# Optimization experiments

Measured on AMD Instinct MI355X. Metric: run time of the kernel, lower is better.

The kernel has to match this reference:

```python
import jax, jax.numpy as jnp
import numpy as np

D_MODEL = 1024
N_HEADS = 16
HEAD_DIM = D_MODEL // N_HEADS


def setup_inputs() -> dict:
    key = jax.random.key(0)
    ks = jax.random.split(key, 9)
    s = 1.0 / np.sqrt(D_MODEL)
    x = jax.random.normal(ks[0], (2, 2048, D_MODEL), dtype=jnp.float32)
    Wq = jax.random.uniform(ks[1], (D_MODEL, D_MODEL), jnp.float32, -s, s)
    bq = jax.random.uniform(ks[2], (D_MODEL,), jnp.float32, -s, s)
    Wk = jax.random.uniform(ks[3], (D_MODEL, D_MODEL), jnp.float32, -s, s)
    bk = jax.random.uniform(ks[4], (D_MODEL,), jnp.float32, -s, s)
    Wv = jax.random.uniform(ks[5], (D_MODEL, D_MODEL), jnp.float32, -s, s)
    bv = jax.random.uniform(ks[6], (D_MODEL,), jnp.float32, -s, s)
    Wo = jax.random.uniform(ks[7], (D_MODEL, D_MODEL), jnp.float32, -s, s)
    bo = jax.random.uniform(ks[8], (D_MODEL,), jnp.float32, -s, s)
    return {"x": x, "Wq": Wq, "bq": bq, "Wk": Wk, "bk": bk,
            "Wv": Wv, "bv": bv, "Wo": Wo, "bo": bo}


def reference(x, Wq, bq, Wk, bk, Wv, bv, Wo, bo):
    B, S, _ = x.shape
    # project and split heads: [B, H, S, Dh]
    def heads(W, b):
        return (x @ W + b).reshape(B, S, N_HEADS, HEAD_DIM).transpose(0, 2, 1, 3)
    Q, K, V = heads(Wq, bq), heads(Wk, bk), heads(Wv, bv)
    scale = 1.0 / np.sqrt(HEAD_DIM).astype(np.float32)
    scores = jnp.einsum('bhsd,bhtd->bhst', Q, K) * scale  # [B,H,S,S]
    causal = jnp.tril(jnp.ones((S, S), dtype=bool))
    scores = jnp.where(causal, scores, -jnp.inf)
    attn = jax.nn.softmax(scores, axis=-1)
    out = jnp.einsum('bhst,bhtd->bhsd', attn, V)  # [B,H,S,Dh]
    out = out.transpose(0, 2, 1, 3).reshape(B, S, D_MODEL)
    return out @ Wo + bo
```

## Files before the change

kernel.cpp:

```cpp
#include <hip/hip_runtime.h>

typedef __attribute__((ext_vector_type(8))) __bf16 bfrag;
typedef __attribute__((ext_vector_type(4))) float f32x4;

#define MFMA(a, b, c) __builtin_amdgcn_mfma_f32_16x16x32_bf16((a), (b), (c), 0, 0, 0)

#define D_MODEL 1024
#define SEQ     2048
#define NB      2
#define NH      16
#define HD      64
#define MROWS   (NB * SEQ)

#define SCALE_LOG2 0.18033688011112043f
#define NEG_BIG    (-3.0e38f)

#define GLOBAL_AS(p) ((const __attribute__((address_space(1))) void*)(p))
#define LDS_AS(p)    ((__attribute__((address_space(3))) void*)(p))
#define ASYNC_CP16(g, l) __builtin_amdgcn_global_load_lds(GLOBAL_AS(g), LDS_AS(l), 16, 0, 0)

__global__ __launch_bounds__(256) void k_prep(
    const float* __restrict__ x,
    const float* __restrict__ Wq, const float* __restrict__ Wk,
    const float* __restrict__ Wv, const float* __restrict__ Wo,
    __bf16* __restrict__ Wt, __bf16* __restrict__ xb)
{
    __shared__ __bf16 t[64][65];
    if (blockIdx.z == 4) {
        size_t base = ((size_t)(blockIdx.y * 16 + blockIdx.x)) * 16384;
        for (int j = 0; j < 8; ++j) {
            size_t i = base + (size_t)j * 2048 + (size_t)threadIdx.x * 8;
            float4 f0 = *(const float4*)&x[i];
            float4 f1 = *(const float4*)&x[i + 4];
            union { uint4 u; __bf16 h[8]; } cv;
            cv.h[0] = (__bf16)f0.x; cv.h[1] = (__bf16)f0.y;
            cv.h[2] = (__bf16)f0.z; cv.h[3] = (__bf16)f0.w;
            cv.h[4] = (__bf16)f1.x; cv.h[5] = (__bf16)f1.y;
            cv.h[6] = (__bf16)f1.z; cv.h[7] = (__bf16)f1.w;
            *(uint4*)&xb[i] = cv.u;
        }
        return;
    }
    const float* src = (blockIdx.z == 0) ? Wq : (blockIdx.z == 1) ? Wk
                      : (blockIdx.z == 2) ? Wv : Wo;
    __bf16* dst = Wt + (size_t)blockIdx.z * (1024u * 1024u);
    int tr = blockIdx.y * 64, tc = blockIdx.x * 64;
    for (int j = 0; j < 16; ++j) {
        int id = threadIdx.x + j * 256;
        int r = id >> 6, c = id & 63;
        t[r][c] = (__bf16)src[(size_t)(tr + r) * 1024 + tc + c];
    }
    __syncthreads();
    for (int j = 0; j < 2; ++j) {
        int id = threadIdx.x + j * 256;
        int r = id >> 3;
        int c8 = (id & 7) * 8;
        union { uint4 u; __bf16 h[8]; } pk;
        for (int i = 0; i < 8; ++i) pk.h[i] = t[c8 + i][r];
        *(uint4*)&dst[(size_t)(tc + r) * 1024 + tr + c8] = pk.u;
    }
}

template <int MODE, bool WT>
__global__ __launch_bounds__(256) void k_gemm128(
    const void* __restrict__ Ap,
    const void* __restrict__ W0, const void* __restrict__ W1,
    const void* __restrict__ W2,
    const float* __restrict__ b0, const float* __restrict__ b1,
    const float* __restrict__ b2, void* __restrict__ dstp)
{
    constexpr int AST = WT ? 64 : 72;
    alignas(16) __shared__ __bf16 SH[18432];
    __bf16* As = SH;
    __bf16* Bs = SH + 128 * AST;

    const int tid = threadIdx.x;
    const int z = blockIdx.z;
    const int m0 = blockIdx.y * 128;
    const int n0 = blockIdx.x * 128;
    const void* W     = (z == 0) ? W0 : (z == 1) ? W1 : W2;
    const float* bias = (z == 0) ? b0 : (z == 1) ? b1 : b2;

    const int wid = tid >> 6, lane = tid & 63;
    const int quad = lane >> 4, l16 = lane & 15;
    const int wRow = (wid >> 1) * 64, wCol = (wid & 1) * 64;

    f32x4 acc[4][4];
    const f32x4 zero = {0.f, 0.f, 0.f, 0.f};
    for (int mi = 0; mi < 4; ++mi)
        for (int ni = 0; ni < 4; ++ni) acc[mi][ni] = zero;

    const int srow = tid >> 3;
    const int sseg = (tid & 7) * 8;
    const int bkrow = tid >> 4;
    const int bnseg = (tid & 15) * 8;
    const int arow = lane >> 3;
    const int akoff = ((lane & 7) * 8) ^ (arow * 8);
    const int sw = (l16 & 7) * 8;

    for (int k0 = 0; k0 < D_MODEL; k0 += 64) {
        __syncthreads();
        if (WT) {
            const __bf16* Ab = (const __bf16*)Ap;
            const __bf16* Bt = (const __bf16*)W;
            for (int it = 0; it < 4; ++it) {
                int row = wid * 32 + it * 8;
                ASYNC_CP16(&Ab[(size_t)(m0 + row + arow) * D_MODEL + k0 + akoff],
                           &As[row * 64]);
                ASYNC_CP16(&Bt[(size_t)(n0 + row + arow) * D_MODEL + k0 + akoff],
                           &Bs[row * 64]);
            }
        } else {
            if (MODE == 0) {
                const float* A = (const float*)Ap;
                for (int it = 0; it < 4; ++it) {
                    int row = srow + it * 32;
                    const float* src = &A[(size_t)(m0 + row) * D_MODEL + k0 + sseg];
                    float4 f0 = *(const float4*)src;
                    float4 f1 = *(const float4*)(src + 4);
                    union { uint4 u; __bf16 h[8]; } cv;
                    cv.h[0] = (__bf16)f0.x; cv.h[1] = (__bf16)f0.y;
                    cv.h[2] = (__bf16)f0.z; cv.h[3] = (__bf16)f0.w;
                    cv.h[4] = (__bf16)f1.x; cv.h[5] = (__bf16)f1.y;
                    cv.h[6] = (__bf16)f1.z; cv.h[7] = (__bf16)f1.w;
                    *(uint4*)&As[row * AST + sseg] = cv.u;
                }
            } else {
                const __bf16* A = (const __bf16*)Ap;
                for (int it = 0; it < 4; ++it) {
                    int row = srow + it * 32;
                    uint4 va = *(const uint4*)&A[(size_t)(m0 + row) * D_MODEL + k0 + sseg];
                    *(uint4*)&As[row * AST + sseg] = va;
                }
            }
            const float* Wf = (const float*)W;
            for (int it = 0; it < 4; ++it) {
                int krow = bkrow + it * 16;
                const float* src = &Wf[(size_t)(k0 + krow) * D_MODEL + n0 + bnseg];
                float4 f0 = *(const float4*)src;
                float4 f1 = *(const float4*)(src + 4);
                Bs[(bnseg + 0) * AST + krow] = (__bf16)f0.x;
                Bs[(bnseg + 1) * AST + krow] = (__bf16)f0.y;
                Bs[(bnseg + 2) * AST + krow] = (__bf16)f0.z;
                Bs[(bnseg + 3) * AST + krow] = (__bf16)f0.w;
                Bs[(bnseg + 4) * AST + krow] = (__bf16)f1.x;
                Bs[(bnseg + 5) * AST + krow] = (__bf16)f1.y;
                Bs[(bnseg + 6) * AST + krow] = (__bf16)f1.z;
                Bs[(bnseg + 7) * AST + krow] = (__bf16)f1.w;
            }
        }
        __syncthreads();
        for (int kk = 0; kk < 64; kk += 32) {
            bfrag af[4], bf[4];
            if (WT) {
                int ko = (kk + quad * 8) ^ sw;
                for (int mi = 0; mi < 4; ++mi)
                    af[mi] = *(const bfrag*)&As[(wRow + mi * 16 + l16) * 64 + ko];
                for (int ni = 0; ni < 4; ++ni)
                    bf[ni] = *(const bfrag*)&Bs[(wCol + ni * 16 + l16) * 64 + ko];
            } else {
                for (int mi = 0; mi < 4; ++mi)
                    af[mi] = *(const bfrag*)&As[(wRow + mi * 16 + l16) * AST + kk + quad * 8];
                for (int ni = 0; ni < 4; ++ni)
                    bf[ni] = *(const bfrag*)&Bs[(wCol + ni * 16 + l16) * AST + kk + quad * 8];
            }
            for (int mi = 0; mi < 4; ++mi)
                for (int ni = 0; ni < 4; ++ni)
                    acc[mi][ni] = MFMA(af[mi], bf[ni], acc[mi][ni]);
        }
    }

    if (MODE == 0) {
        float biasv[4];
        for (int ni = 0; ni < 4; ++ni) biasv[ni] = bias[n0 + wCol + ni * 16 + l16];
        const int b = m0 >> 11, m0s = m0 & 2047, h0 = n0 >> 6;
        __syncthreads();
        if (z < 2) {
            for (int mi = 0; mi < 4; ++mi)
                for (int ni = 0; ni < 4; ++ni) {
                    int col = wCol + ni * 16 + l16;
                    for (int r = 0; r < 4; ++r) {
                        float v = acc[mi][ni][r] + biasv[ni];
                        if (z == 0) v *= SCALE_LOG2;
                        SH[(wRow + mi * 16 + quad * 4 + r) * 136 + col] = (__bf16)v;
                    }
                }
            __syncthreads();
            __bf16* qk = (__bf16*)dstp + (size_t)z * (MROWS * (size_t)D_MODEL);
            for (int i = 0; i < 8; ++i) {
                int rid = i * 32 + (tid >> 3);
                int hl = rid >> 7, sl = rid & 127;
                int dcol = (tid & 7) * 8;
                uint4 v = *(const uint4*)&SH[sl * 136 + hl * 64 + dcol];
                *(uint4*)&qk[(((size_t)b * NH + h0 + hl) * SEQ + m0s + sl) * HD + dcol] = v;
            }
        } else {
            for (int mi = 0; mi < 4; ++mi)
                for (int ni = 0; ni < 4; ++ni) {
                    int col = wCol + ni * 16 + l16;
                    int s0 = wRow + mi * 16 + quad * 4;
                    union { unsigned long long u; __bf16 h4[4]; } pk;
                    for (int r = 0; r < 4; ++r)
                        pk.h4[r] = (__bf16)(acc[mi][ni][r] + biasv[ni]);
                    *(unsigned long long*)&SH[col * 136 + s0] = pk.u;
                }
            __syncthreads();
            __bf16* vv = (__bf16*)dstp + (size_t)2 * (MROWS * (size_t)D_MODEL);
            for (int i = 0; i < 8; ++i) {
                int rid = i * 16 + (tid >> 4);
                int hl = rid >> 6, d = rid & 63;
                int sc = (tid & 15) * 8;
                uint4 v = *(const uint4*)&SH[rid * 136 + sc];
                *(uint4*)&vv[(((size_t)b * NH + h0 + hl) * HD + d) * SEQ + m0s + sc] = v;
            }
        }
    } else {
        for (int mi = 0; mi < 4; ++mi)
            for (int ni = 0; ni < 4; ++ni) {
                int gn = n0 + wCol + ni * 16 + l16;
                float bv = bias[gn];
                for (int r = 0; r < 4; ++r) {
                    int gm = m0 + wRow + mi * 16 + quad * 4 + r;
                    ((float*)dstp)[(size_t)gm * D_MODEL + gn] = acc[mi][ni][r] + bv;
                }
            }
    }
}

__global__ __launch_bounds__(256) void k_gemm_out(
    const __bf16* __restrict__ A, const __bf16* __restrict__ Bt,
    const float* __restrict__ bias, float* __restrict__ dst)
{
    alignas(16) __shared__ __bf16 As[64 * 64];
    alignas(16) __shared__ __bf16 Bs[128 * 64];

    const int tid = threadIdx.x;
    const int m0 = blockIdx.y * 64;
    const int n0 = blockIdx.x * 128;
    const int wid = tid >> 6, lane = tid & 63;
    const int quad = lane >> 4, l16 = lane & 15;
    const int wRow = (wid >> 1) * 32, wCol = (wid & 1) * 64;

    f32x4 acc[2][4];
    const f32x4 zero = {0.f, 0.f, 0.f, 0.f};
    for (int mi = 0; mi < 2; ++mi)
        for (int ni = 0; ni < 4; ++ni) acc[mi][ni] = zero;

    const int arow = lane >> 3;
    const int akoff = ((lane & 7) * 8) ^ (arow * 8);
    const int sw = (l16 & 7) * 8;

    for (int k0 = 0; k0 < D_MODEL; k0 += 64) {
        __syncthreads();
        for (int it = 0; it < 2; ++it) {
            int row = wid * 16 + it * 8;
            ASYNC_CP16(&A[(size_t)(m0 + row + arow) * D_MODEL + k0 + akoff],
                       &As[row * 64]);
        }
        for (int it = 0; it < 4; ++it) {
            int row = wid * 32 + it * 8;
            ASYNC_CP16(&Bt[(size_t)(n0 + row + arow) * D_MODEL + k0 + akoff],
                       &Bs[row * 64]);
        }
        __syncthreads();
        for (int kk = 0; kk < 64; kk += 32) {
            int ko = (kk + quad * 8) ^ sw;
            bfrag af[2], bf[4];
            for (int mi = 0; mi < 2; ++mi)
                af[mi] = *(const bfrag*)&As[(wRow + mi * 16 + l16) * 64 + ko];
            for (int ni = 0; ni < 4; ++ni)
                bf[ni] = *(const bfrag*)&Bs[(wCol + ni * 16 + l16) * 64 + ko];
            for (int mi = 0; mi < 2; ++mi)
                for (int ni = 0; ni < 4; ++ni)
                    acc[mi][ni] = MFMA(af[mi], bf[ni], acc[mi][ni]);
        }
    }

    for (int mi = 0; mi < 2; ++mi)
        for (int ni = 0; ni < 4; ++ni) {
            int gn = n0 + wCol + ni * 16 + l16;
            float bv = bias[gn];
            for (int r = 0; r < 4; ++r) {
                int gm = m0 + wRow + mi * 16 + quad * 4 + r;
                dst[(size_t)gm * D_MODEL + gn] = acc[mi][ni][r] + bv;
            }
        }
}

__global__ __launch_bounds__(256) void k_attn(
    const __bf16* __restrict__ Q, const __bf16* __restrict__ K,
    const __bf16* __restrict__ Vt, __bf16* __restrict__ O)
{
    alignas(16) __shared__ __bf16 Ks[64 * 64];
    alignas(16) __shared__ __bf16 Vts[64 * 64];
    alignas(16) __shared__ __bf16 Ps[4][16 * 64];

    const int tid = threadIdx.x, wid = tid >> 6, lane = tid & 63;
    const int quad = lane >> 4, l16 = lane & 15;
    const int u = (blockIdx.x + blockIdx.y + 16 * blockIdx.z) & 31;
    const int qb = (u & 1) ? 31 - (u >> 1) : (u >> 1);
    const int h = blockIdx.y, b = blockIdx.z;
    const size_t bh = ((size_t)b * NH + h) * SEQ * HD;
    const __bf16* Qg  = Q + bh + (size_t)qb * 64 * HD;
    const __bf16* Kg  = K + bh;
    const __bf16* Vtg = Vt + ((size_t)b * NH + h) * HD * SEQ;

    bfrag qf[2];
    qf[0] = *(const bfrag*)&Qg[(size_t)(wid * 16 + l16) * HD + quad * 8];
    qf[1] = *(const bfrag*)&Qg[(size_t)(wid * 16 + l16) * HD + 32 + quad * 8];

    const f32x4 zero = {0.f, 0.f, 0.f, 0.f};
    f32x4 o[4];
    for (int dt = 0; dt < 4; ++dt) o[dt] = zero;
    float lrow = 0.f;
    const int q = qb * 64 + wid * 16 + l16;
    const int srcbase = (lane & 48) + quad * 4;
    const int sw = (l16 & 7) * 8;
    const int ntile = qb + 1;

    const int row0 = tid >> 3, seg = (tid & 7) * 8;
    const int sseg = seg ^ ((row0 & 7) * 8);

    uint4 kreg0 = *(const uint4*)&Kg[(size_t)row0 * HD + seg];
    uint4 kreg1 = *(const uint4*)&Kg[(size_t)(row0 + 32) * HD + seg];
    uint4 vreg0 = *(const uint4*)&Vtg[(size_t)row0 * SEQ + seg];
    uint4 vreg1 = *(const uint4*)&Vtg[(size_t)(row0 + 32) * SEQ + seg];

    for (int t = 0; t < ntile; ++t) {
        const int j0 = t * 64;
        __syncthreads();
        *(uint4*)&Ks[row0 * 64 + sseg] = kreg0;
        *(uint4*)&Ks[(row0 + 32) * 64 + sseg] = kreg1;
        *(uint4*)&Vts[row0 * 64 + sseg] = vreg0;
        *(uint4*)&Vts[(row0 + 32) * 64 + sseg] = vreg1;
        if (t + 1 < ntile) {
            const int j1 = j0 + 64;
            kreg0 = *(const uint4*)&Kg[(size_t)(j1 + row0) * HD + seg];
            kreg1 = *(const uint4*)&Kg[(size_t)(j1 + row0 + 32) * HD + seg];
            vreg0 = *(const uint4*)&Vtg[(size_t)row0 * SEQ + j1 + seg];
            vreg1 = *(const uint4*)&Vtg[(size_t)(row0 + 32) * SEQ + j1 + seg];
        }
        __syncthreads();

        f32x4 st[4];
        for (int kt = 0; kt < 4; ++kt) {
            bfrag ka0 = *(const bfrag*)&Ks[(kt * 16 + l16) * 64 + ((quad * 8) ^ sw)];
            bfrag ka1 = *(const bfrag*)&Ks[(kt * 16 + l16) * 64 + ((32 + quad * 8) ^ sw)];
            st[kt] = MFMA(ka1, qf[1], MFMA(ka0, qf[0], zero));
        }

        if (t == ntile - 1) {
            for (int kt = 0; kt < 4; ++kt)
                for (int r = 0; r < 4; ++r) {
                    float v = (j0 + kt * 16 + quad * 4 + r > q) ? NEG_BIG : st[kt][r];
                    float p = exp2f(v);
                    st[kt][r] = p;
                    lrow += p;
                }
        } else {
            for (int kt = 0; kt < 4; ++kt)
                for (int r = 0; r < 4; ++r) {
                    float p = exp2f(st[kt][r]);
                    st[kt][r] = p;
                    lrow += p;
                }
        }

        for (int kt = 0; kt < 4; ++kt) {
            union { unsigned long long u; __bf16 h4[4]; } pk;
            for (int r = 0; r < 4; ++r) pk.h4[r] = (__bf16)st[kt][r];
            *(unsigned long long*)&Ps[wid][l16 * 64 + ((kt * 16 + quad * 4) ^ sw)] = pk.u;
        }
        asm volatile("s_waitcnt lgkmcnt(0)" ::: "memory");

        for (int c = 0; c < 2; ++c) {
            int ko = (c * 32 + quad * 8) ^ sw;
            bfrag pf = *(const bfrag*)&Ps[wid][l16 * 64 + ko];
            for (int dt = 0; dt < 4; ++dt) {
                bfrag vf = *(const bfrag*)&Vts[(dt * 16 + l16) * 64 + ko];
                o[dt] = MFMA(pf, vf, o[dt]);
            }
        }
    }

    float lsum = lrow + __shfl_xor(lrow, 16, 64);
    lsum = lsum + __shfl_xor(lsum, 32, 64);
    for (int r = 0; r < 4; ++r) {
        float lr = __shfl(lsum, srcbase + r, 64);
        float inv = 1.0f / lr;
        size_t base = ((size_t)b * SEQ + qb * 64 + wid * 16 + quad * 4 + r) * D_MODEL
                    + (size_t)h * HD;
        for (int dt = 0; dt < 4; ++dt)
            O[base + dt * 16 + l16] = (__bf16)(o[dt][r] * inv);
    }
}

extern "C" void kernel_launch(void* const* d_in, const int* in_sizes, int n_in,
                              void* d_out, int out_size, void* d_ws, size_t ws_size,
                              hipStream_t stream)
{
    const float* x  = (const float*)d_in[0];
    const float* Wq = (const float*)d_in[1];
    const float* bq = (const float*)d_in[2];
    const float* Wk = (const float*)d_in[3];
    const float* bk = (const float*)d_in[4];
    const float* Wv = (const float*)d_in[5];
    const float* bv = (const float*)d_in[6];
    const float* Wo = (const float*)d_in[7];
    const float* bo = (const float*)d_in[8];

    __bf16* ws = (__bf16*)d_ws;
    const size_t M1 = 1024u * 1024u;
    __bf16* qkv    = ws;
    __bf16* attn_o = ws + 12 * M1;
    __bf16* Wt     = ws + 16 * M1;
    __bf16* xb     = ws + 20 * M1;

    const bool fast = ws_size >= (size_t)48 * 1024 * 1024;

    if (fast) {
        k_prep<<<dim3(16, 16, 5), 256, 0, stream>>>(x, Wq, Wk, Wv, Wo, Wt, xb);
        k_gemm128<0, true><<<dim3(8, 32, 3), 256, 0, stream>>>(
            xb, Wt, Wt + M1, Wt + 2 * M1, bq, bk, bv, qkv);
        k_attn<<<dim3(32, 16, 2), 256, 0, stream>>>(
            qkv, qkv + 4 * M1, qkv + 8 * M1, attn_o);
        k_gemm_out<<<dim3(8, 64), 256, 0, stream>>>(
            attn_o, Wt + 3 * M1, bo, (float*)d_out);
    } else {
        k_gemm128<0, false><<<dim3(8, 32, 3), 256, 0, stream>>>(
            x, Wq, Wk, Wv, bq, bk, bv, qkv);
        k_attn<<<dim3(32, 16, 2), 256, 0, stream>>>(
            qkv, qkv + 4 * M1, qkv + 8 * M1, attn_o);
        k_gemm128<1, false><<<dim3(8, 32, 1), 256, 0, stream>>>(
            attn_o, Wo, Wo, Wo, bo, bo, bo, (float*)d_out);
    }
}
```

Measured before the change: 198.2 us.

## Vectorize weight prep loads, swizzle GEMM tile order, compute softmax sums via MFMA

```diff
diff --git a/kernel.cpp b/kernel.cpp
--- a/kernel.cpp
+++ b/kernel.cpp
@@ -45,10 +45,13 @@
                       : (blockIdx.z == 2) ? Wv : Wo;
     __bf16* dst = Wt + (size_t)blockIdx.z * (1024u * 1024u);
     int tr = blockIdx.y * 64, tc = blockIdx.x * 64;
-    for (int j = 0; j < 16; ++j) {
+    for (int j = 0; j < 4; ++j) {
         int id = threadIdx.x + j * 256;
-        int r = id >> 6, c = id & 63;
-        t[r][c] = (__bf16)src[(size_t)(tr + r) * 1024 + tc + c];
+        int r = id >> 4;
+        int c4 = (id & 15) * 4;
+        float4 f = *(const float4*)&src[(size_t)(tr + r) * 1024 + tc + c4];
+        t[r][c4 + 0] = (__bf16)f.x; t[r][c4 + 1] = (__bf16)f.y;
+        t[r][c4 + 2] = (__bf16)f.z; t[r][c4 + 3] = (__bf16)f.w;
     }
     __syncthreads();
     for (int j = 0; j < 2; ++j) {
@@ -76,8 +79,11 @@
 
     const int tid = threadIdx.x;
     const int z = blockIdx.z;
-    const int m0 = blockIdx.y * 128;
-    const int n0 = blockIdx.x * 128;
+    const int lid = blockIdx.x + (blockIdx.y << 3);
+    const int mt = ((lid & 7) << 2) + ((lid >> 3) >> 3);
+    const int nt = (lid >> 3) & 7;
+    const int m0 = mt * 128;
+    const int n0 = nt * 128;
     const void* W     = (z == 0) ? W0 : (z == 1) ? W1 : W2;
     const float* bias = (z == 0) ? b0 : (z == 1) ? b1 : b2;
 
@@ -235,8 +241,11 @@
     alignas(16) __shared__ __bf16 Bs[128 * 64];
 
     const int tid = threadIdx.x;
-    const int m0 = blockIdx.y * 64;
-    const int n0 = blockIdx.x * 128;
+    const int lid = blockIdx.x + (blockIdx.y << 3);
+    const int mt = ((lid & 7) << 3) + ((lid >> 3) >> 3);
+    const int nt = (lid >> 3) & 7;
+    const int m0 = mt * 64;
+    const int n0 = nt * 128;
     const int wid = tid >> 6, lane = tid & 63;
     const int quad = lane >> 4, l16 = lane & 15;
     const int wRow = (wid >> 1) * 32, wCol = (wid & 1) * 64;
@@ -309,12 +318,15 @@
     qf[0] = *(const bfrag*)&Qg[(size_t)(wid * 16 + l16) * HD + quad * 8];
     qf[1] = *(const bfrag*)&Qg[(size_t)(wid * 16 + l16) * HD + 32 + quad * 8];
 
+    union { uint4 u; bfrag f; } onesu;
+    onesu.u = make_uint4(0x3F803F80u, 0x3F803F80u, 0x3F803F80u, 0x3F803F80u);
+    const bfrag onesf = onesu.f;
+
     const f32x4 zero = {0.f, 0.f, 0.f, 0.f};
     f32x4 o[4];
     for (int dt = 0; dt < 4; ++dt) o[dt] = zero;
-    float lrow = 0.f;
+    f32x4 o_l = zero;
     const int q = qb * 64 + wid * 16 + l16;
-    const int srcbase = (lane & 48) + quad * 4;
     const int sw = (l16 & 7) * 8;
     const int ntile = qb + 1;
 
@@ -353,17 +365,12 @@
             for (int kt = 0; kt < 4; ++kt)
                 for (int r = 0; r < 4; ++r) {
                     float v = (j0 + kt * 16 + quad * 4 + r > q) ? NEG_BIG : st[kt][r];
-                    float p = exp2f(v);
-                    st[kt][r] = p;
-                    lrow += p;
+                    st[kt][r] = exp2f(v);
                 }
         } else {
             for (int kt = 0; kt < 4; ++kt)
-                for (int r = 0; r < 4; ++r) {
-                    float p = exp2f(st[kt][r]);
-                    st[kt][r] = p;
-                    lrow += p;
-                }
+                for (int r = 0; r < 4; ++r)
+                    st[kt][r] = exp2f(st[kt][r]);
         }
 
         for (int kt = 0; kt < 4; ++kt) {
@@ -380,14 +387,12 @@
                 bfrag vf = *(const bfrag*)&Vts[(dt * 16 + l16) * 64 + ko];
                 o[dt] = MFMA(pf, vf, o[dt]);
             }
-        }
-    }
-
-    float lsum = lrow + __shfl_xor(lrow, 16, 64);
-    lsum = lsum + __shfl_xor(lsum, 32, 64);
+            o_l = MFMA(pf, onesf, o_l);
+        }
+    }
+
     for (int r = 0; r < 4; ++r) {
-        float lr = __shfl(lsum, srcbase + r, 64);
-        float inv = 1.0f / lr;
+        float inv = 1.0f / o_l[r];
         size_t base = ((size_t)b * SEQ + qb * 64 + wid * 16 + quad * 4 + r) * D_MODEL
                     + (size_t)h * HD;
         for (int dt = 0; dt < 4; ++dt)
```

Result: no change. 196.6 us (-0.8%).
